# Performance work log

Hardware: AMD Instinct MI355X
Metric: run time of the kernel (lower is better)

The kernel has to match this reference:

```python
import jax, jax.numpy as jnp
import numpy as np

N = 100000   # nodes
E = 300000   # edges (avg degree ~3, molecular graphs)
DIN = 128    # input node features
H = 512      # hidden
OUT = 256    # out_channels
G = 4096     # number of graphs
EPS = 1e-5
SLOPE = 0.01  # LeakyReLU default negative slope
SELF_W = 2.0  # improved=True self-loop weight


def setup_inputs() -> dict:
    key = jax.random.key(0)
    ks = jax.random.split(key, 12)
    x = jax.random.normal(ks[0], (N, DIN), dtype=jnp.float32)
    edge_index = jax.random.randint(ks[1], (2, E), 0, N, dtype=jnp.int64)
    batch = jnp.sort(jax.random.randint(ks[2], (N,), 0, G, dtype=jnp.int64))
    s1 = 1.0 / np.sqrt(DIN)
    s2 = 1.0 / np.sqrt(H)
    return {
        "x": x,
        "edge_index": edge_index,
        "batch": batch,
        "W1": jax.random.normal(ks[3], (DIN, H), dtype=jnp.float32) * s1,
        "b1": jax.random.normal(ks[4], (H,), dtype=jnp.float32) * 0.01,
        "g1": jax.random.uniform(ks[5], (H,), dtype=jnp.float32, minval=0.5, maxval=1.5),
        "beta1": jax.random.normal(ks[6], (H,), dtype=jnp.float32) * 0.01,
        "W2": jax.random.normal(ks[7], (H, H), dtype=jnp.float32) * s2,
        "b2": jax.random.normal(ks[8], (H,), dtype=jnp.float32) * 0.01,
        "g2": jax.random.uniform(ks[9], (H,), dtype=jnp.float32, minval=0.5, maxval=1.5),
        "beta2": jax.random.normal(ks[10], (H,), dtype=jnp.float32) * 0.01,
        "Wf": jax.random.normal(ks[11], (H, OUT), dtype=jnp.float32) * s2,
        "bf": jnp.zeros((OUT,), dtype=jnp.float32),
    }


def _gcn_conv(x, W, b, row, col, n):
    # GCNConv(improved=True, add_self_loops=True, normalize=True), edge_weight=None
    h = x @ W                                   # [n, H]
    ones = jnp.ones(row.shape[0], dtype=h.dtype)
    deg = jax.ops.segment_sum(ones, col, num_segments=n) + SELF_W
    dinv = jax.lax.rsqrt(deg)                   # deg > 0 always (self-loop weight 2)
    norm = dinv[row] * dinv[col]                # [E]
    agg = jax.ops.segment_sum(h[row] * norm[:, None], col, num_segments=n)
    agg = agg + h * (SELF_W * dinv * dinv)[:, None]  # self-loop messages, no edge materialization
    return agg + b


def _bn(x, g, beta):
    # training-mode BatchNorm1d: biased batch stats
    mu = jnp.mean(x, axis=0)
    var = jnp.mean(jnp.square(x - mu), axis=0)
    return g * (x - mu) * jax.lax.rsqrt(var + EPS) + beta


def reference(x, edge_index, batch, W1, b1, g1, beta1, W2, b2, g2, beta2, Wf, bf):
    row, col = edge_index[0], edge_index[1]
    n = x.shape[0]
    h = _gcn_conv(x, W1, b1, row, col, n)
    h = jax.nn.leaky_relu(_bn(h, g1, beta1), SLOPE)
    # dropout is identity in eval mode
    h = _gcn_conv(h, W2, b2, row, col, n)
    h = jax.nn.leaky_relu(_bn(h, g2, beta2), SLOPE)
    pooled = jax.ops.segment_max(h, batch, num_segments=G)
    pooled = jnp.where(jnp.isfinite(pooled), pooled, 0.0)  # empty graphs -> 0 (torch_scatter fill)
    return pooled @ Wf + bf
```

## Files before the change

kernel.cpp:

```cpp
#include <hip/hip_runtime.h>
#include <hip/hip_bf16.h>

typedef __hip_bfloat16 bf16;
typedef __attribute__((ext_vector_type(8))) short short8;
typedef __attribute__((ext_vector_type(4))) float f32x4;

#define HDIM 512
#define SLOPE 0.01f
#define BN_EPS 1e-5f
#define STRIPES 8

__device__ inline float bf2f(short s) {
    unsigned u = ((unsigned)(unsigned short)s) << 16;
    return __builtin_bit_cast(float, u);
}
__device__ inline unsigned short f2bfbits(float v) {
    bf16 h = __float2bfloat16(v);
    return (unsigned short)__builtin_bit_cast(short, h);
}

struct EdgeRec { int src; float nm; };

__global__ void detect_types(const int* __restrict__ ei, const unsigned* __restrict__ xw,
                             int* __restrict__ flags, float* __restrict__ gpart) {
    __shared__ int nzhi, okbf;
    if (threadIdx.x == 0) { nzhi = 0; okbf = 0; }
    __syncthreads();
    int lo = 0, ok = 0;
    for (int i = threadIdx.x; i < 2048; i += 256)
        if (ei[2 * i + 1] != 0) lo++;
    for (int i = threadIdx.x; i < 1024; i += 256) {
        unsigned w = (xw[i] & 0xFFFFu) << 16;
        float av = fabsf(__builtin_bit_cast(float, w));
        if (av > 0.0009f && av < 64.0f) ok++;
    }
    for (int i = threadIdx.x; i < STRIPES * 2 * HDIM; i += 256) gpart[i] = 0.f;
    if (lo) atomicAdd(&nzhi, lo);
    if (ok) atomicAdd(&okbf, ok);
    __syncthreads();
    if (threadIdx.x == 0) {
        flags[0] = (nzhi == 0) ? 1 : 0;
        flags[1] = (okbf < 512) ? 1 : 0;
    }
}

__global__ void conv_all_idx(const int* __restrict__ ei, const int* __restrict__ batch,
                             int* __restrict__ ei32, int* __restrict__ batch32,
                             int* __restrict__ cnt, int e2, int n,
                             const int* __restrict__ flags) {
    int i = blockIdx.x * blockDim.x + threadIdx.x;
    int i64 = flags[0];
    if (i < e2) {
        int v = i64 ? (int)((const long long*)ei)[i] : ei[i];
        ei32[i] = v;
        if (i >= e2 / 2) atomicAdd(&cnt[v], 1);
    } else if (i < e2 + n) {
        int j = i - e2;
        batch32[j] = i64 ? (int)((const long long*)batch)[j] : batch[j];
    }
}

__global__ void wt_conv_all(const void* __restrict__ W1, const void* __restrict__ W2,
                            const void* __restrict__ Wf, const void* __restrict__ bf_,
                            bf16* __restrict__ W1T, bf16* __restrict__ W2T,
                            bf16* __restrict__ WfT, bf16* __restrict__ bfbf,
                            const int* __restrict__ flags) {
    const int S1 = 128 * 512, S2 = 512 * 512, S3 = 512 * 256;
    int idx = blockIdx.x * 256 + threadIdx.x;
    bool f32 = flags[1] != 0;
    if (idx < S1) {
        int nn = idx / 128, k = idx - nn * 128;
        float v = f32 ? ((const float*)W1)[(size_t)k * 512 + nn]
                      : __bfloat162float(((const bf16*)W1)[(size_t)k * 512 + nn]);
        W1T[idx] = __float2bfloat16(v);
    } else if (idx < S1 + S2) {
        int t = idx - S1;
        int nn = t / 512, k = t - nn * 512;
        float v = f32 ? ((const float*)W2)[(size_t)k * 512 + nn]
                      : __bfloat162float(((const bf16*)W2)[(size_t)k * 512 + nn]);
        W2T[t] = __float2bfloat16(v);
    } else if (idx < S1 + S2 + S3) {
        int t = idx - S1 - S2;
        int nn = t / 512, k = t - nn * 512;
        float v = f32 ? ((const float*)Wf)[(size_t)k * 256 + nn]
                      : __bfloat162float(((const bf16*)Wf)[(size_t)k * 256 + nn]);
        WfT[t] = __float2bfloat16(v);
    } else if (idx < S1 + S2 + S3 + 256) {
        int t = idx - S1 - S2 - S3;
        float v = f32 ? ((const float*)bf_)[t]
                      : __bfloat162float(((const bf16*)bf_)[t]);
        bfbf[t] = __float2bfloat16(v);
    }
}

__global__ void finalize_deg(const int* __restrict__ cnt, float* __restrict__ dinv,
                             float* __restrict__ selfw, int n) {
    int i = blockIdx.x * blockDim.x + threadIdx.x;
    if (i < n) {
        float d = (float)cnt[i] + 2.0f;
        dinv[i] = rsqrtf(d);
        selfw[i] = 2.0f / d;
    }
}

__global__ __launch_bounds__(256) void scan_part(
    const int* __restrict__ counts, int* __restrict__ offsets,
    int* __restrict__ bsum, int n)
{
    __shared__ int s[512];
    int b = blockIdx.x;
    int base = b * 512;
    int t = threadIdx.x;
    s[t]       = (base + t       < n) ? counts[base + t]       : 0;
    s[t + 256] = (base + t + 256 < n) ? counts[base + t + 256] : 0;

    int offset = 1;
    for (int d = 256; d > 0; d >>= 1) {
        __syncthreads();
        if (t < d) {
            int ai = offset * (2 * t + 1) - 1;
            int bi = offset * (2 * t + 2) - 1;
            s[bi] += s[ai];
        }
        offset <<= 1;
    }
    __syncthreads();
    if (t == 0) { bsum[b] = s[511]; s[511] = 0; }
    for (int d = 1; d < 512; d <<= 1) {
        offset >>= 1;
        __syncthreads();
        if (t < d) {
            int ai = offset * (2 * t + 1) - 1;
            int bi = offset * (2 * t + 2) - 1;
            int tmp = s[ai]; s[ai] = s[bi]; s[bi] += tmp;
        }
    }
    __syncthreads();
    if (base + t < n)       offsets[base + t]       = s[t];
    if (base + t + 256 < n) offsets[base + t + 256] = s[t + 256];
}

__global__ __launch_bounds__(1024) void scan_tops(int* __restrict__ bsum, int nb) {
    __shared__ int s[1024];
    int t = threadIdx.x;
    s[t] = (t < nb) ? bsum[t] : 0;
    __syncthreads();
    for (int off = 1; off < 1024; off <<= 1) {
        int v = (t >= off) ? s[t - off] : 0;
        __syncthreads();
        s[t] += v;
        __syncthreads();
    }
    if (t < nb) bsum[t] = (t == 0) ? 0 : s[t - 1];
}

__global__ __launch_bounds__(256) void scan_add(
    int* __restrict__ offsets, const int* __restrict__ bsum, int n, int e)
{
    int b = blockIdx.x;
    int base = b * 512;
    int add = bsum[b];
    int t = threadIdx.x;
    if (base + t < n)       offsets[base + t]       += add;
    if (base + t + 256 < n) offsets[base + t + 256] += add;
    if (b == 0 && t == 0) offsets[n] = e;
}

__global__ void scatter_edges(const int* __restrict__ rows, const int* __restrict__ cols,
                              const int* __restrict__ offsets, int* __restrict__ cursor,
                              const float* __restrict__ dinv,
                              EdgeRec* __restrict__ er, int e)
{
    int i = blockIdx.x * blockDim.x + threadIdx.x;
    if (i < e) {
        int d = cols[i];
        int r = rows[i];
        int pos = offsets[d] + atomicAdd(&cursor[d], 1);
        EdgeRec rec;
        rec.src = r;
        rec.nm = dinv[d] * dinv[r];
        er[pos] = rec;
    }
}

template<bool STATS>
__global__ __launch_bounds__(256, 4) void gemm_m97(
    const bf16* __restrict__ A, const bf16* __restrict__ BT,
    void* __restrict__ C, const bf16* __restrict__ bias,
    int M, int K, int N, const int* __restrict__ cf32,
    float* __restrict__ gpart, int MB)
{
    __shared__ bf16 As[128 * 32];
    __shared__ bf16 Bs[128 * 32];
    __shared__ float ssum[STATS ? 128 : 1];
    __shared__ float ssq[STATS ? 128 : 1];

    int NBN = N >> 7;
    int id = blockIdx.x;
    int grp = id / (8 * NBN);
    int loc = id - grp * 8 * NBN;
    int mi = loc & 7;
    int nblk = loc >> 3;
    int mblk = grp * 8 + mi;
    if (mblk >= MB) return;

    int tid = threadIdx.x;
    int wave = tid >> 6, lane = tid & 63, q = lane >> 4, r = lane & 15;
    int wm = (wave >> 1) * 64, wn = (wave & 1) * 64;
    int m0 = mblk * 128, n0 = nblk * 128;
    bool c32 = cf32 && *cf32;

    if constexpr (STATS) {
        if (tid < 128) { ssum[tid] = 0.f; ssq[tid] = 0.f; }
    }

    int lrow = lane >> 2;
    int lcol = (((lane & 3) ^ ((lane >> 3) & 3)) * 8);
    int aoff = (q ^ ((r >> 1) & 3)) * 8;

    f32x4 acc[4][4];
#pragma unroll
    for (int mi2 = 0; mi2 < 4; mi2++)
#pragma unroll
        for (int ni = 0; ni < 4; ni++)
            acc[mi2][ni] = {0.f, 0.f, 0.f, 0.f};

    for (int k0 = 0; k0 < K; k0 += 32) {
#pragma unroll
        for (int i = 0; i < 2; i++) {
            int c = wave * 2 + i;
            const bf16* ga = A  + (size_t)(m0 + c * 16 + lrow) * K + k0 + lcol;
            const bf16* gb = BT + (size_t)(n0 + c * 16 + lrow) * K + k0 + lcol;
            __builtin_amdgcn_global_load_lds(
                (const __attribute__((address_space(1))) unsigned*)ga,
                (__attribute__((address_space(3))) unsigned*)(As + c * 512), 16, 0, 0);
            __builtin_amdgcn_global_load_lds(
                (const __attribute__((address_space(1))) unsigned*)gb,
                (__attribute__((address_space(3))) unsigned*)(Bs + c * 512), 16, 0, 0);
        }
        __syncthreads();

        short8 a[4], b[4];
#pragma unroll
        for (int mi2 = 0; mi2 < 4; mi2++) a[mi2] = *(const short8*)&As[(wm + mi2 * 16 + r) * 32 + aoff];
#pragma unroll
        for (int ni = 0; ni < 4; ni++) b[ni] = *(const short8*)&Bs[(wn + ni * 16 + r) * 32 + aoff];
#pragma unroll
        for (int mi2 = 0; mi2 < 4; mi2++)
#pragma unroll
            for (int ni = 0; ni < 4; ni++)
                acc[mi2][ni] = __builtin_amdgcn_mfma_f32_16x16x32_bf16(a[mi2], b[ni], acc[mi2][ni], 0, 0, 0);
        __syncthreads();
    }

#pragma unroll
    for (int mi2 = 0; mi2 < 4; mi2++) {
#pragma unroll
        for (int ni = 0; ni < 4; ni++) {
            int gn = n0 + wn + ni * 16 + r;
            float bv = bias ? __bfloat162float(bias[gn]) : 0.f;
#pragma unroll
            for (int reg = 0; reg < 4; reg++) {
                int gm = m0 + wm + mi2 * 16 + q * 4 + reg;
                if (gm < M) {
                    float val = acc[mi2][ni][reg] + bv;
                    if (c32) ((float*)C)[(size_t)gm * N + gn] = val;
                    else     ((bf16*)C)[(size_t)gm * N + gn] = __float2bfloat16(val);
                }
            }
        }
    }

    if constexpr (STATS) {
#pragma unroll
        for (int ni = 0; ni < 4; ni++) {
            float cs = 0.f, cq = 0.f;
#pragma unroll
            for (int mi2 = 0; mi2 < 4; mi2++)
#pragma unroll
                for (int reg = 0; reg < 4; reg++) {
                    int gm = m0 + wm + mi2 * 16 + q * 4 + reg;
                    if (gm < M) {
                        float v = acc[mi2][ni][reg];
                        cs += v; cq += v * v;
                    }
                }
            int c = wn + ni * 16 + r;
            atomicAdd(&ssum[c], cs);
            atomicAdd(&ssq[c], cq);
        }
        __syncthreads();
        if (tid < 128) {
            float* base = gpart + (size_t)(mblk & (STRIPES - 1)) * 2 * HDIM;
            atomicAdd(&base[n0 + tid], ssum[tid]);
            atomicAdd(&base[HDIM + n0 + tid], ssq[tid]);
        }
    }
}

__global__ __launch_bounds__(256) void agg_csr_din(
    const void* __restrict__ x, const int* __restrict__ offsets,
    const EdgeRec* __restrict__ er, const float* __restrict__ selfw,
    bf16* __restrict__ out, int n, const int* __restrict__ flags)
{
    int wave = threadIdx.x >> 6, lane = threadIdx.x & 63;
    int gw = blockIdx.x * 4 + wave;
    int nw = gridDim.x * 4;
    bool f32 = flags[1] != 0;

    for (int dst = gw; dst < n; dst += nw) {
        int s0 = offsets[dst], s1 = offsets[dst + 1];
        float sw = selfw[dst];
        float a0, a1;
        if (f32) {
            float2 v = ((const float2*)x)[(size_t)dst * 64 + lane];
            a0 = sw * v.x; a1 = sw * v.y;
        } else {
            unsigned u = ((const unsigned*)x)[(size_t)dst * 64 + lane];
            a0 = sw * bf2f((short)(u & 0xFFFF)); a1 = sw * bf2f((short)(u >> 16));
        }
        int p = s0;
        for (; p + 1 < s1; p += 2) {
            EdgeRec e0 = er[p], e1 = er[p + 1];
            if (f32) {
                float2 v0 = ((const float2*)x)[(size_t)e0.src * 64 + lane];
                float2 v1 = ((const float2*)x)[(size_t)e1.src * 64 + lane];
                a0 += e0.nm * v0.x + e1.nm * v1.x;
                a1 += e0.nm * v0.y + e1.nm * v1.y;
            } else {
                unsigned u0 = ((const unsigned*)x)[(size_t)e0.src * 64 + lane];
                unsigned u1 = ((const unsigned*)x)[(size_t)e1.src * 64 + lane];
                a0 += e0.nm * bf2f((short)(u0 & 0xFFFF)) + e1.nm * bf2f((short)(u1 & 0xFFFF));
                a1 += e0.nm * bf2f((short)(u0 >> 16))    + e1.nm * bf2f((short)(u1 >> 16));
            }
        }
        if (p < s1) {
            EdgeRec e0 = er[p];
            if (f32) {
                float2 v0 = ((const float2*)x)[(size_t)e0.src * 64 + lane];
                a0 += e0.nm * v0.x; a1 += e0.nm * v0.y;
            } else {
                unsigned u0 = ((const unsigned*)x)[(size_t)e0.src * 64 + lane];
                a0 += e0.nm * bf2f((short)(u0 & 0xFFFF)); a1 += e0.nm * bf2f((short)(u0 >> 16));
            }
        }
        ((unsigned*)out)[(size_t)dst * 64 + lane] =
            (unsigned)f2bfbits(a0) | ((unsigned)f2bfbits(a1) << 16);
    }
}

__global__ __launch_bounds__(256) void agg_csr_bn(
    const bf16* __restrict__ h, const int* __restrict__ offsets,
    const EdgeRec* __restrict__ er, const float* __restrict__ selfw,
    const float* __restrict__ scale, const float* __restrict__ shift,
    bf16* __restrict__ y, int n)
{
    int wave = threadIdx.x >> 6, lane = threadIdx.x & 63;
    int f0 = lane * 8;
    int gw = blockIdx.x * 4 + wave;
    int nw = gridDim.x * 4;

    float sc[8], sh[8];
#pragma unroll
    for (int j = 0; j < 8; j++) { sc[j] = scale[f0 + j]; sh[j] = shift[f0 + j]; }

    for (int dst = gw; dst < n; dst += nw) {
        int s0 = offsets[dst], s1 = offsets[dst + 1];
        float sw = selfw[dst];
        short8 hv = *(const short8*)(h + (size_t)dst * HDIM + f0);
        float acc[8];
#pragma unroll
        for (int j = 0; j < 8; j++) {
            float t = sc[j] * bf2f(hv[j]) + sh[j];
            t = t > 0.f ? t : SLOPE * t;
            acc[j] = sw * t;
        }
        int p = s0;
        for (; p + 1 < s1; p += 2) {
            EdgeRec e0 = er[p], e1 = er[p + 1];
            short8 v0 = *(const short8*)(h + (size_t)e0.src * HDIM + f0);
            short8 v1 = *(const short8*)(h + (size_t)e1.src * HDIM + f0);
#pragma unroll
            for (int j = 0; j < 8; j++) {
                float t0 = sc[j] * bf2f(v0[j]) + sh[j];
                t0 = t0 > 0.f ? t0 : SLOPE * t0;
                float t1 = sc[j] * bf2f(v1[j]) + sh[j];
                t1 = t1 > 0.f ? t1 : SLOPE * t1;
                acc[j] += e0.nm * t0 + e1.nm * t1;
            }
        }
        if (p < s1) {
            EdgeRec e0 = er[p];
            short8 v0 = *(const short8*)(h + (size_t)e0.src * HDIM + f0);
#pragma unroll
            for (int j = 0; j < 8; j++) {
                float t0 = sc[j] * bf2f(v0[j]) + sh[j];
                t0 = t0 > 0.f ? t0 : SLOPE * t0;
                acc[j] += e0.nm * t0;
            }
        }
        short8 o;
#pragma unroll
        for (int j = 0; j < 8; j++) ((bf16*)&o)[j] = __float2bfloat16(acc[j]);
        *(short8*)(y + (size_t)dst * HDIM + f0) = o;
    }
}

__global__ void bn_final(float* __restrict__ gpart,
                         const void* __restrict__ gamma, const void* __restrict__ beta,
                         float* __restrict__ scale, float* __restrict__ shift,
                         float invN, const int* __restrict__ flags)
{
    int f = threadIdx.x;
    float s = 0.f, q = 0.f;
#pragma unroll
    for (int k = 0; k < STRIPES; k++) {
        s += gpart[(size_t)k * 2 * HDIM + f];
        q += gpart[(size_t)k * 2 * HDIM + HDIM + f];
        gpart[(size_t)k * 2 * HDIM + f] = 0.f;
        gpart[(size_t)k * 2 * HDIM + HDIM + f] = 0.f;
    }
    float g = flags[1] ? ((const float*)gamma)[f]
                       : __bfloat162float(((const bf16*)gamma)[f]);
    float b = flags[1] ? ((const float*)beta)[f]
                       : __bfloat162float(((const bf16*)beta)[f]);
    float mu = s * invN;
    float var = fmaxf(q * invN - mu * mu, 0.f);
    float inv = rsqrtf(var + BN_EPS);
    float sc = g * inv;
    scale[f] = sc;
    shift[f] = b - mu * sc;
}

__global__ __launch_bounds__(256) void pool_fused(
    const bf16* __restrict__ y, const int* __restrict__ batch,
    const float* __restrict__ scale, const float* __restrict__ shift,
    bf16* __restrict__ pooled, int n, int G)
{
    int wave = threadIdx.x >> 6, lane = threadIdx.x & 63;
    int g = blockIdx.x * 4 + wave;
    if (g >= G) return;
    int f0 = lane * 8;

    int lo = 0, hi = n;
    while (lo < hi) { int mid = (lo + hi) >> 1; if (batch[mid] < g) lo = mid + 1; else hi = mid; }
    int s = lo;
    hi = n;
    while (lo < hi) { int mid = (lo + hi) >> 1; if (batch[mid] <= g) lo = mid + 1; else hi = mid; }
    int e = lo;

    float mx[8], mn[8];
#pragma unroll
    for (int j = 0; j < 8; j++) { mx[j] = -3.0e38f; mn[j] = 3.0e38f; }

    int rr = s;
    for (; rr + 1 < e; rr += 2) {
        short8 v0 = *(const short8*)(y + (size_t)rr * HDIM + f0);
        short8 v1 = *(const short8*)(y + (size_t)(rr + 1) * HDIM + f0);
#pragma unroll
        for (int j = 0; j < 8; j++) {
            float a = bf2f(v0[j]), b = bf2f(v1[j]);
            mx[j] = fmaxf(mx[j], fmaxf(a, b));
            mn[j] = fminf(mn[j], fminf(a, b));
        }
    }
    if (rr < e) {
        short8 v0 = *(const short8*)(y + (size_t)rr * HDIM + f0);
#pragma unroll
        for (int j = 0; j < 8; j++) {
            float a = bf2f(v0[j]);
            mx[j] = fmaxf(mx[j], a);
            mn[j] = fminf(mn[j], a);
        }
    }

    short8 o;
#pragma unroll
    for (int j = 0; j < 8; j++) {
        float outv = 0.f;
        if (s < e) {
            float sc = scale[f0 + j];
            float t = sc * (sc >= 0.f ? mx[j] : mn[j]) + shift[f0 + j];
            outv = t > 0.f ? t : SLOPE * t;
        }
        ((bf16*)&o)[j] = __float2bfloat16(outv);
    }
    *(short8*)(pooled + (size_t)g * HDIM + f0) = o;
}

extern "C" void kernel_launch(void* const* d_in, const int* in_sizes, int n_in,
                              void* d_out, int out_size, void* d_ws, size_t ws_size,
                              hipStream_t stream)
{
    const void* x     = d_in[0];
    const int*  ei    = (const int*)d_in[1];
    const int*  batch = (const int*)d_in[2];

    const int N   = in_sizes[2];
    const int E   = in_sizes[1] / 2;
    const int DIN = 128;
    const int OUT = 256;
    const int G   = out_size / OUT;
    const int Mp  = (N + 127) & ~127;
    const int MB  = Mp / 128;
    const int MB8 = (MB + 7) & ~7;

    char* p = (char*)d_ws;
    bf16* B1     = (bf16*)p;  p += (size_t)Mp * HDIM * sizeof(bf16);
    bf16* B2     = (bf16*)p;  p += (size_t)Mp * HDIM * sizeof(bf16);
    bf16* Q      = (bf16*)p;  p += (size_t)Mp * DIN * sizeof(bf16);
    bf16* W1T    = (bf16*)p;  p += (size_t)HDIM * DIN * sizeof(bf16);
    bf16* W2T    = (bf16*)p;  p += (size_t)HDIM * HDIM * sizeof(bf16);
    bf16* WfT    = (bf16*)p;  p += (size_t)OUT * HDIM * sizeof(bf16);
    bf16* bfbf   = (bf16*)p;  p += 512 * sizeof(bf16);
    int* ei32    = (int*)p;   p += (size_t)2 * E * sizeof(int);
    int* batch32 = (int*)p;   p += (size_t)N * sizeof(int);
    float* dinv  = (float*)p; p += (size_t)N * sizeof(float);
    float* selfw = (float*)p; p += (size_t)N * sizeof(float);
    int* offsets = (int*)p;   p += (size_t)(N + 4) * sizeof(int);
    int* cursor  = (int*)p;   p += (size_t)N * sizeof(int);
    EdgeRec* er  = (EdgeRec*)p; p += (size_t)E * sizeof(EdgeRec);
    int* bsum    = (int*)p;   p += 1024 * sizeof(int);
    float* gpart = (float*)p; p += (size_t)STRIPES * 2 * HDIM * sizeof(float);
    float* sc1   = (float*)p; p += HDIM * sizeof(float);
    float* sh1   = (float*)p; p += HDIM * sizeof(float);
    float* sc2   = (float*)p; p += HDIM * sizeof(float);
    float* sh2   = (float*)p; p += HDIM * sizeof(float);
    int* flags   = (int*)p;   p += 4 * sizeof(int);

    detect_types<<<1, 256, 0, stream>>>(ei, (const unsigned*)x, flags, gpart);
    hipMemsetAsync(cursor, 0, (size_t)N * sizeof(int), stream);
    conv_all_idx<<<(2 * E + N + 255) / 256, 256, 0, stream>>>(
        ei, batch, ei32, batch32, cursor, 2 * E, N, flags);
    wt_conv_all<<<(128 * 512 + 512 * 512 + 512 * 256 + 256 + 255) / 256, 256, 0, stream>>>(
        d_in[3], d_in[7], d_in[11], d_in[12], W1T, W2T, WfT, bfbf, flags);

    const int* rows = ei32;
    const int* cols = ei32 + E;

    finalize_deg<<<(N + 255) / 256, 256, 0, stream>>>(cursor, dinv, selfw, N);
    int nb = (N + 511) / 512;
    scan_part<<<nb, 256, 0, stream>>>(cursor, offsets, bsum, N);
    scan_tops<<<1, 1024, 0, stream>>>(bsum, nb);
    scan_add<<<nb, 256, 0, stream>>>(offsets, bsum, N, E);
    hipMemsetAsync(cursor, 0, (size_t)N * sizeof(int), stream);
    scatter_edges<<<(E + 255) / 256, 256, 0, stream>>>(rows, cols, offsets, cursor,
                                                       dinv, er, E);

    int gemm_blocks = MB8 * (HDIM / 128);

    agg_csr_din<<<2048, 256, 0, stream>>>(x, offsets, er, selfw, Q, N, flags);
    gemm_m97<true><<<gemm_blocks, 256, 0, stream>>>(
        Q, W1T, B2, nullptr, N, DIN, HDIM, nullptr, gpart, MB);
    bn_final<<<1, HDIM, 0, stream>>>(gpart, d_in[5], d_in[6], sc1, sh1, 1.0f / N, flags);

    agg_csr_bn<<<2048, 256, 0, stream>>>(B2, offsets, er, selfw, sc1, sh1, B1, N);
    gemm_m97<true><<<gemm_blocks, 256, 0, stream>>>(
        B1, W2T, B2, nullptr, N, HDIM, HDIM, nullptr, gpart, MB);
    bn_final<<<1, HDIM, 0, stream>>>(gpart, d_in[9], d_in[10], sc2, sh2, 1.0f / N, flags);

    pool_fused<<<(G + 3) / 4, 256, 0, stream>>>(B2, batch32, sc2, sh2, Q, N, G);
    gemm_m97<false><<<(G / 128) * (OUT / 128), 256, 0, stream>>>(
        Q, WfT, d_out, bfbf, G, HDIM, OUT, flags + 1, nullptr, G / 128);
}
```

Baseline: 518.5 us.

## Double-buffer GEMM LDS tiles and reduce BN stats via wave shuffles

The GEMM main loop now uses two LDS buffers, issuing the global-to-LDS load for the next K tile before computing on the current one, which removes one barrier per iteration and overlaps load latency with MFMA work. The BatchNorm statistics epilogue drops the shared-memory atomic reduction and block barrier. It instead reduces across quads with xor shuffles and issues global atomics directly from each wave. This doubles LDS usage, which may limit occupancy, and roughly doubles the global atomics per block since two wave rows now hit each column.

```diff
diff --git a/kernel.cpp b/kernel.cpp
--- a/kernel.cpp
+++ b/kernel.cpp
@@ -183,6 +183,39 @@
     }
 }
 
+#define GEMM_STAGE(buf, kk)                                                              \
+    {                                                                                    \
+        _Pragma("unroll")                                                                \
+        for (int i_ = 0; i_ < 2; i_++) {                                                 \
+            int c_ = wave * 2 + i_;                                                      \
+            const bf16* ga_ = A  + (size_t)(m0 + c_ * 16 + lrow) * K + (kk) + lcol;      \
+            const bf16* gb_ = BT + (size_t)(n0 + c_ * 16 + lrow) * K + (kk) + lcol;      \
+            __builtin_amdgcn_global_load_lds(                                            \
+                (const __attribute__((address_space(1))) unsigned*)ga_,                  \
+                (__attribute__((address_space(3))) unsigned*)(As[buf] + c_ * 512), 16, 0, 0); \
+            __builtin_amdgcn_global_load_lds(                                            \
+                (const __attribute__((address_space(1))) unsigned*)gb_,                  \
+                (__attribute__((address_space(3))) unsigned*)(Bs[buf] + c_ * 512), 16, 0, 0); \
+        }                                                                                \
+    }
+
+#define GEMM_COMPUTE(buf)                                                                \
+    {                                                                                    \
+        short8 a[4], b[4];                                                               \
+        _Pragma("unroll")                                                                \
+        for (int mi2 = 0; mi2 < 4; mi2++)                                                \
+            a[mi2] = *(const short8*)&As[buf][(wm + mi2 * 16 + r) * 32 + aoff];          \
+        _Pragma("unroll")                                                                \
+        for (int ni = 0; ni < 4; ni++)                                                   \
+            b[ni] = *(const short8*)&Bs[buf][(wn + ni * 16 + r) * 32 + aoff];            \
+        _Pragma("unroll")                                                                \
+        for (int mi2 = 0; mi2 < 4; mi2++)                                                \
+            _Pragma("unroll")                                                            \
+            for (int ni = 0; ni < 4; ni++)                                               \
+                acc[mi2][ni] = __builtin_amdgcn_mfma_f32_16x16x32_bf16(                  \
+                    a[mi2], b[ni], acc[mi2][ni], 0, 0, 0);                               \
+    }
+
 template<bool STATS>
 __global__ __launch_bounds__(256, 4) void gemm_m97(
     const bf16* __restrict__ A, const bf16* __restrict__ BT,
@@ -190,10 +223,8 @@
     int M, int K, int N, const int* __restrict__ cf32,
     float* __restrict__ gpart, int MB)
 {
-    __shared__ bf16 As[128 * 32];
-    __shared__ bf16 Bs[128 * 32];
-    __shared__ float ssum[STATS ? 128 : 1];
-    __shared__ float ssq[STATS ? 128 : 1];
+    __shared__ bf16 As[2][128 * 32];
+    __shared__ bf16 Bs[2][128 * 32];
 
     int NBN = N >> 7;
     int id = blockIdx.x;
@@ -210,10 +241,6 @@
     int m0 = mblk * 128, n0 = nblk * 128;
     bool c32 = cf32 && *cf32;
 
-    if constexpr (STATS) {
-        if (tid < 128) { ssum[tid] = 0.f; ssq[tid] = 0.f; }
-    }
-
     int lrow = lane >> 2;
     int lcol = (((lane & 3) ^ ((lane >> 3) & 3)) * 8);
     int aoff = (q ^ ((r >> 1) & 3)) * 8;
@@ -225,33 +252,19 @@
         for (int ni = 0; ni < 4; ni++)
             acc[mi2][ni] = {0.f, 0.f, 0.f, 0.f};
 
-    for (int k0 = 0; k0 < K; k0 += 32) {
-#pragma unroll
-        for (int i = 0; i < 2; i++) {
-            int c = wave * 2 + i;
-            const bf16* ga = A  + (size_t)(m0 + c * 16 + lrow) * K + k0 + lcol;
-            const bf16* gb = BT + (size_t)(n0 + c * 16 + lrow) * K + k0 + lcol;
-            __builtin_amdgcn_global_load_lds(
-                (const __attribute__((address_space(1))) unsigned*)ga,
-                (__attribute__((address_space(3))) unsigned*)(As + c * 512), 16, 0, 0);
-            __builtin_amdgcn_global_load_lds(
-                (const __attribute__((address_space(1))) unsigned*)gb,
-                (__attribute__((address_space(3))) unsigned*)(Bs + c * 512), 16, 0, 0);
-        }
+    const int nK = K >> 5;
+
+    GEMM_STAGE(0, 0);
+    __syncthreads();
+
+    int cur = 0;
+    for (int t = 1; t < nK; ++t) {
+        GEMM_STAGE(cur ^ 1, t * 32);
+        GEMM_COMPUTE(cur);
         __syncthreads();
-
-        short8 a[4], b[4];
-#pragma unroll
-        for (int mi2 = 0; mi2 < 4; mi2++) a[mi2] = *(const short8*)&As[(wm + mi2 * 16 + r) * 32 + aoff];
-#pragma unroll
-        for (int ni = 0; ni < 4; ni++) b[ni] = *(const short8*)&Bs[(wn + ni * 16 + r) * 32 + aoff];
-#pragma unroll
-        for (int mi2 = 0; mi2 < 4; mi2++)
-#pragma unroll
-            for (int ni = 0; ni < 4; ni++)
-                acc[mi2][ni] = __builtin_amdgcn_mfma_f32_16x16x32_bf16(a[mi2], b[ni], acc[mi2][ni], 0, 0, 0);
-        __syncthreads();
-    }
+        cur ^= 1;
+    }
+    GEMM_COMPUTE(cur);
 
 #pragma unroll
     for (int mi2 = 0; mi2 < 4; mi2++) {
@@ -272,6 +285,7 @@
     }
 
     if constexpr (STATS) {
+        float* base = gpart + (size_t)(mblk & (STRIPES - 1)) * 2 * HDIM;
 #pragma unroll
         for (int ni = 0; ni < 4; ni++) {
             float cs = 0.f, cq = 0.f;
@@ -285,15 +299,15 @@
                         cs += v; cq += v * v;
                     }
                 }
-            int c = wn + ni * 16 + r;
-            atomicAdd(&ssum[c], cs);
-            atomicAdd(&ssq[c], cq);
-        }
-        __syncthreads();
-        if (tid < 128) {
-            float* base = gpart + (size_t)(mblk & (STRIPES - 1)) * 2 * HDIM;
-            atomicAdd(&base[n0 + tid], ssum[tid]);
-            atomicAdd(&base[HDIM + n0 + tid], ssq[tid]);
+            cs += __shfl_xor(cs, 16, 64);
+            cs += __shfl_xor(cs, 32, 64);
+            cq += __shfl_xor(cq, 16, 64);
+            cq += __shfl_xor(cq, 32, 64);
+            if (q == 0) {
+                int c = n0 + wn + ni * 16 + r;
+                atomicAdd(&base[c], cs);
+                atomicAdd(&base[HDIM + c], cq);
+            }
         }
     }
 }
```

Result: faster. 472.0 us (-9.0%).
